# Performance work log

Measured on AMD Instinct MI355X. Metric: run time of the kernel, lower is better.

The kernel has to match this reference:

```python
import jax, jax.numpy as jnp
import numpy as np

D_MODEL = 1024
N_HEADS = 16
D_K = D_MODEL // N_HEADS
THETA = 10000.0
B, S = 2, 2048


def setup_inputs() -> dict:
    key = jax.random.key(0)
    ks = jax.random.split(key, 5)
    sigma = 2.0 / (D_MODEL + D_MODEL) ** 0.5
    x = jax.random.normal(ks[0], (B, S, D_MODEL), dtype=jnp.float32)
    Wq = jax.random.normal(ks[1], (D_MODEL, D_MODEL), dtype=jnp.float32) * sigma
    Wk = jax.random.normal(ks[2], (D_MODEL, D_MODEL), dtype=jnp.float32) * sigma
    Wv = jax.random.normal(ks[3], (D_MODEL, D_MODEL), dtype=jnp.float32) * sigma
    Wo = jax.random.normal(ks[4], (D_MODEL, D_MODEL), dtype=jnp.float32) * sigma
    token_positions = jnp.arange(S, dtype=jnp.int64 if jax.config.read('jax_enable_x64') else jnp.int32)
    return {"x": x, "Wq": Wq, "Wk": Wk, "Wv": Wv, "Wo": Wo, "token_positions": token_positions}


def _apply_rope(t, token_positions):
    # t: (H, B, S, D_K); token_positions: (S,) broadcasts over leading dims
    half = D_K // 2
    inv_freq = 1.0 / (THETA ** (jnp.arange(0, D_K, 2, dtype=jnp.float32) / D_K))  # (half,)
    ang = token_positions.astype(jnp.float32)[..., None] * inv_freq              # (S, half)
    cos, sin = jnp.cos(ang), jnp.sin(ang)
    t2 = t.reshape(*t.shape[:-1], half, 2)  # interleaved pairs
    o0 = t2[..., 0] * cos - t2[..., 1] * sin
    o1 = t2[..., 0] * sin + t2[..., 1] * cos
    return jnp.stack((o0, o1), axis=-1).reshape(t.shape)


def _split_heads(t):
    # (B, S, D_MODEL) -> (H, B, S, D_K)
    Bb, Ss, _ = t.shape
    return jnp.moveaxis(t.reshape(Bb, Ss, N_HEADS, D_K), 2, 0)


def reference(x, Wq, Wk, Wv, Wo, token_positions):
    Q = _split_heads(jnp.einsum('oi,bsi->bso', Wq, x))
    K = _split_heads(jnp.einsum('oi,bsi->bso', Wk, x))
    V = _split_heads(jnp.einsum('oi,bsi->bso', Wv, x))
    Q = _apply_rope(Q, token_positions)
    K = _apply_rope(K, token_positions)
    scores = jnp.einsum('hbqd,hbkd->hbqk', Q, K) * (D_K ** -0.5)  # (H,B,S,S)
    causal = jnp.tril(jnp.ones((S, S), dtype=bool))
    scores = jnp.where(causal, scores, -jnp.inf)
    attn = jax.nn.softmax(scores, axis=-1)
    out = jnp.einsum('hbqk,hbkd->hbqd', attn, V)  # (H,B,S,D_K)
    out = jnp.moveaxis(out, 0, 2).reshape(x.shape[0], x.shape[1], D_MODEL)
    return jnp.einsum('oi,bsi->bso', Wo, out)
```

## Files before the change

### kernel.cpp

```cpp
#include <hip/hip_runtime.h>

#define DM 1024
#define NH 16
#define DK 64
#define BB 2
#define SS 2048

typedef unsigned short u16;
typedef unsigned int   u32;
typedef __bf16 bf16x8 __attribute__((ext_vector_type(8)));
typedef float  f32x4  __attribute__((ext_vector_type(4)));
typedef float  f32x16 __attribute__((ext_vector_type(16)));

__device__ __forceinline__ u16 f2bf(float f){
  u32 u = __float_as_uint(f);
  u32 r = (u + 0x7FFFu + ((u >> 16) & 1u)) >> 16;
  return (u16)r;
}
__device__ __forceinline__ float bf2f(u16 v){ return __uint_as_float(((u32)v) << 16); }

__device__ __forceinline__ u32 cvtpk(float lo, float hi){
  u32 r;
  asm volatile("v_cvt_pk_bf16_f32 %0, %1, %2" : "=v"(r) : "v"(lo), "v"(hi));
  return r;
}

__device__ __forceinline__ void gl16(const void* g, void* l){
  __builtin_amdgcn_global_load_lds((const __attribute__((address_space(1))) u32*)g,
                                   (__attribute__((address_space(3))) u32*)l, 16, 0, 0);
}
__device__ __forceinline__ f32x4 mfma16(bf16x8 a, bf16x8 b, f32x4 c){
  return __builtin_amdgcn_mfma_f32_16x16x32_bf16(a, b, c, 0, 0, 0);
}
__device__ __forceinline__ f32x16 mfma32(bf16x8 a, bf16x8 b, f32x16 c){
  return __builtin_amdgcn_mfma_f32_32x32x16_bf16(a, b, c, 0, 0, 0);
}

__global__ void k_cast(const float* __restrict__ x,  const float* __restrict__ wq,
                       const float* __restrict__ wk, const float* __restrict__ wv,
                       const float* __restrict__ wo, u16* __restrict__ xb,
                       u16* __restrict__ wb, float* __restrict__ tab){
  if (blockIdx.x >= 8192){
    int e = (blockIdx.x - 8192)*256 + threadIdx.x;
    int p = e >> 5, j = e & 31;
    float s, c;
    sincosf((float)p * exp2f(-0.4152410118609203f * (float)j), &s, &c);
    float2 v; v.x = c; v.y = s;
    *(float2*)(tab + e*2) = v;
    return;
  }
  int e = blockIdx.x*1024 + threadIdx.x*4;
  int r = e >> 20;
  const float* s; u16* d; int local;
  if (r < 4){ s = x; d = xb; local = e; }
  else {
    const float* ws[4] = {wq, wk, wv, wo};
    int w = r - 4;
    local = e & 0xFFFFF;
    s = ws[w]; d = wb + ((size_t)w << 20);
  }
  float4 v = *(const float4*)(s + local);
  uint2 t; t.x = cvtpk(v.x, v.y); t.y = cvtpk(v.z, v.w);
  *(uint2*)(d + local) = t;
}

__device__ __forceinline__ int xcd_swz(int lin, int nwg){
  return (lin & 7) * (nwg >> 3) + (lin >> 3);
}

template<bool SWAP>
__device__ __forceinline__ void gemm_core(const u16* __restrict__ A, const u16* __restrict__ Bw,
                                          u16* S, f32x4 (&acc)[4][4], int m0, int n0){
  const int tid = threadIdx.x, lane = tid & 63, wid = tid >> 6;
  const int wm = (wid >> 1) * 64, wn = (wid & 1) * 64;
  const int ql = lane & 15, lg = lane >> 4;

  #define STAGE_G(buf, k0)                                                       \
    _Pragma("unroll")                                                            \
    for (int i = 0; i < 4; i++){                                                 \
      int L = i*4096 + tid*16;                                                   \
      int r_ = L >> 7;                                                           \
      int orig = ((L >> 4) & 7) ^ (r_ & 7);                                      \
      const u16* src = (orig < 4)                                                \
          ? (A  + (size_t)(m0 + r_)*DM + (k0) + orig*8)                          \
          : (Bw + (size_t)(n0 + r_)*DM + (k0) + (orig - 4)*8);                   \
      gl16(src, (char*)(buf) + L);                                               \
    }

  #define COMPUTE_T(buf)                                                         \
    {                                                                            \
      bf16x8 af[4], bfr[4];                                                      \
      _Pragma("unroll")                                                          \
      for (int mi = 0; mi < 4; mi++){                                            \
        int r = wm + mi*16 + ql;                                                 \
        af[mi] = *(const bf16x8*)((char*)(buf) + r*128 + ((lg*16) ^ ((r & 7) << 4))); \
      }                                                                          \
      _Pragma("unroll")                                                          \
      for (int ni = 0; ni < 4; ni++){                                            \
        int r = wn + ni*16 + ql;                                                 \
        bfr[ni] = *(const bf16x8*)((char*)(buf) + r*128 + ((64 + lg*16) ^ ((r & 7) << 4))); \
      }                                                                          \
      __builtin_amdgcn_s_setprio(1);                                             \
      _Pragma("unroll")                                                          \
      for (int mi = 0; mi < 4; mi++)                                             \
        _Pragma("unroll")                                                        \
        for (int ni = 0; ni < 4; ni++)                                           \
          acc[mi][ni] = SWAP ? mfma16(bfr[ni], af[mi], acc[mi][ni])              \
                             : mfma16(af[mi], bfr[ni], acc[mi][ni]);             \
      __builtin_amdgcn_s_setprio(0);                                             \
    }

  char* b0 = (char*)S;
  char* b1 = (char*)S + 16384;
  char* b2 = (char*)S + 32768;

  STAGE_G(b0, 0);
  STAGE_G(b1, 32);

  #pragma unroll 3
  for (int t = 0; t < 30; t++){
    asm volatile("s_waitcnt vmcnt(4)" ::: "memory");
    __builtin_amdgcn_s_barrier();
    STAGE_G(b2, (t+2)*32);
    COMPUTE_T(b0);
    char* tmp = b0; b0 = b1; b1 = b2; b2 = tmp;
  }
  asm volatile("s_waitcnt vmcnt(4)" ::: "memory");
  __builtin_amdgcn_s_barrier();
  COMPUTE_T(b0);
  { char* tmp = b0; b0 = b1; b1 = b2; b2 = tmp; }
  asm volatile("s_waitcnt vmcnt(0)" ::: "memory");
  __builtin_amdgcn_s_barrier();
  COMPUTE_T(b0);

  #undef STAGE_G
  #undef COMPUTE_T
}

__global__ __launch_bounds__(256) void k_gemm_qkv(const u16* __restrict__ xb, const u16* __restrict__ Wb,
                                                  u16* __restrict__ Qb, u16* __restrict__ Kb,
                                                  u16* __restrict__ Vt_g, const int* __restrict__ pos,
                                                  const float* __restrict__ tab){
  __shared__ __align__(16) u16 S[3*8192];
  int lin = (int)blockIdx.x + 8*((int)blockIdx.y + 32*(int)blockIdx.z);
  lin = xcd_swz(lin, 768);
  const int bx = lin & 7, by = (lin >> 3) & 31, z = lin >> 8;
  const int m0 = by * 128, n0 = bx * 128;

  const u16* Bw = Wb + ((size_t)z << 20);
  f32x4 acc[4][4] = {};
  gemm_core<true>(xb, Bw, S, acc, m0, n0);
  const int lane = threadIdx.x & 63, wid = threadIdx.x >> 6;
  const int wm0 = m0 + (wid >> 1)*64, wn0 = n0 + (wid & 1)*64;
  const int ql = lane & 15, lg = lane >> 4;

  if (z == 2){
    #pragma unroll
    for (int mi = 0; mi < 4; mi++){
      const int mrow = wm0 + mi*16 + ql;
      const int bq = mrow >> 11, sq = mrow & (SS-1);
      u16* vt = Vt_g + ((size_t)bq*NH*DK)*SS + sq;
      #pragma unroll
      for (int ni = 0; ni < 4; ni++){
        const int nb = wn0 + ni*16 + lg*4;
        #pragma unroll
        for (int r = 0; r < 4; r++)
          vt[(size_t)(nb + r)*SS] = f2bf(acc[mi][ni][r]);
      }
    }
    return;
  }

  u16* C = (z == 0) ? Qb : Kb;
  const float4* tab4 = (const float4*)tab;
  #pragma unroll
  for (int mi = 0; mi < 4; mi++){
    const int mrow = wm0 + mi*16 + ql;
    const int p = pos[mrow & (SS-1)];
    #pragma unroll
    for (int ni = 0; ni < 4; ni++){
      const int nb = wn0 + ni*16 + lg*4;
      float o0 = acc[mi][ni][0], o1 = acc[mi][ni][1];
      float o2 = acc[mi][ni][2], o3 = acc[mi][ni][3];
      int j0 = (nb >> 1) & 31;
      float4 cs = tab4[p*16 + (j0 >> 1)];
      float t0 = o0*cs.x - o1*cs.y, t1 = o0*cs.y + o1*cs.x;
      o0 = t0; o1 = t1;
      t0 = o2*cs.z - o3*cs.w; t1 = o2*cs.w + o3*cs.z;
      o2 = t0; o3 = t1;
      uint2 w; w.x = cvtpk(o0, o1); w.y = cvtpk(o2, o3);
      *(uint2*)(C + (size_t)mrow*DM + nb) = w;
    }
  }
}

__global__ __launch_bounds__(256) void k_gemm_out(const u16* __restrict__ AO, const u16* __restrict__ Wo,
                                                  float* __restrict__ Co){
  __shared__ __align__(16) u16 S[3*8192];
  int lin = (int)blockIdx.x + 8*(int)blockIdx.y;
  lin = xcd_swz(lin, 256);
  const int bx = lin & 7, by = lin >> 3;
  const int m0 = by * 128, n0 = bx * 128;

  f32x4 acc[4][4] = {};
  gemm_core<false>(AO, Wo, S, acc, m0, n0);
  const int lane = threadIdx.x & 63, wid = threadIdx.x >> 6;
  const int wm0 = m0 + (wid >> 1)*64, wn0 = n0 + (wid & 1)*64;
  #pragma unroll
  for (int mi = 0; mi < 4; mi++)
    #pragma unroll
    for (int ni = 0; ni < 4; ni++)
      #pragma unroll
      for (int r = 0; r < 4; r++){
        int m = wm0 + mi*16 + (lane >> 4)*4 + r;
        int n = wn0 + ni*16 + (lane & 15);
        Co[(size_t)m*DM + n] = acc[mi][ni][r];
      }
}

__global__ __launch_bounds__(512, 4) void k_attn(const u16* __restrict__ Q, const u16* __restrict__ K,
                                                 const u16* __restrict__ Vt_g, u16* __restrict__ AO){
  __shared__ __align__(16) u16 Ks[4][64*64];
  __shared__ __align__(16) u16 Vt[4][64*64];
  const int tid = threadIdx.x, lane = tid & 63, wid = tid >> 6;
  const int b = blockIdx.z, h = blockIdx.y;
  const int qb = b ? (15 - (int)blockIdx.x) : (int)blockIdx.x;
  const int strip = wid & 3, g = wid >> 2;
  const int qw = qb*128 + strip*32;
  const size_t base = ((size_t)b*SS)*DM + (size_t)h*DK;
  const size_t vtb  = ((size_t)b*NH + h)*DK*SS;
  const int qi = lane & 31, hh = lane >> 5;
  const int NI = qb + 1;
  const float SC = 0.18033688011112042f;
  const float THR = 8.0f / SC;
  const int qm15 = (qi & 15) << 4;

  const u16* qptr = Q + base + (size_t)(qw + qi)*DM + hh*8;
  bf16x8 qf0 = *(const bf16x8*)(qptr);
  bf16x8 qf1 = *(const bf16x8*)(qptr + 16);
  bf16x8 qf2 = *(const bf16x8*)(qptr + 32);
  bf16x8 qf3 = *(const bf16x8*)(qptr + 48);

  const int L = tid*16;
  const int Lm = ((L >> 3) & 0xF0) ^ ((L >> 6) & 0x10);
  const int A_ = L ^ Lm;
  const int srow = A_ >> 7;
  const int scol = (A_ & 127) >> 1;

  #define STAGE1(bi, t)                                                          \
    {                                                                             \
      const int kn0_ = (t)*64;                                                    \
      gl16(K    + base + (size_t)(kn0_ + srow)*DM + scol, (char*)Ks[bi] + L);      \
      gl16(Vt_g + vtb  + (size_t)srow*SS + kn0_ + scol, (char*)Vt[bi] + L);        \
    }

  STAGE1(0, 0); STAGE1(1, 1);
  if (NI > 1){
    STAGE1(2, 2); STAGE1(3, 3);
    asm volatile("s_waitcnt vmcnt(4)" ::: "memory");
  } else {
    asm volatile("s_waitcnt vmcnt(0)" ::: "memory");
  }
  __builtin_amdgcn_s_barrier();

  f32x16 oacc0 = {}, oacc1 = {};
  float m = -3e38f, lsum = 0.f;

  for (int k = 0; k < NI; k++){
    const int t = 2*k + g;
    const int kv0 = t*64;
    const int bsel = ((k & 1) << 1) | g;
    const char* kb = (const char*)Ks[bsel];
    const char* vb = (const char*)Vt[bsel];

    if (kv0 <= qw + 31){
      f32x16 sf0 = {}, sf1 = {};
      __builtin_amdgcn_s_setprio(1);
      #pragma unroll
      for (int kc = 0; kc < 4; kc++){
        const int co = kc*32 + hh*16;
        const int a0 = (qi*128 + co) ^ qm15;
        bf16x8 kfa = *(const bf16x8*)(kb + a0);
        bf16x8 kfb = *(const bf16x8*)(kb + a0 + 4096);
        bf16x8 qf = (kc == 0) ? qf0 : (kc == 1) ? qf1 : (kc == 2) ? qf2 : qf3;
        sf0 = mfma32(kfa, qf, sf0);
        sf1 = mfma32(kfb, qf, sf1);
      }
      __builtin_amdgcn_s_setprio(0);

      if (kv0 + 63 > qw){
        const int qa = qw + qi;
        #pragma unroll
        for (int r = 0; r < 16; r++){
          int rowoff = (r & 3) + 8*(r >> 2) + 4*hh;
          sf0[r] = (kv0 + rowoff      <= qa) ? sf0[r] : -3e38f;
          sf1[r] = (kv0 + 32 + rowoff <= qa) ? sf1[r] : -3e38f;
        }
      }

      float mx = -3e38f;
      #pragma unroll
      for (int r = 0; r < 16; r++) mx = fmaxf(mx, fmaxf(sf0[r], sf1[r]));
      if (!__all(mx <= m + THR)){
        mx = fmaxf(mx, __shfl_xor(mx, 32));
        const float mn = fmaxf(m, mx);
        const float alpha = exp2f((m - mn)*SC);
        oacc0 *= alpha; oacc1 *= alpha; lsum *= alpha;
        m = mn;
      }

      const float nms = -m*SC;
      float psum = 0.f;
      #pragma unroll
      for (int r = 0; r < 16; r++){
        sf0[r] = exp2f(fmaf(sf0[r], SC, nms));
        sf1[r] = exp2f(fmaf(sf1[r], SC, nms));
        psum += sf0[r] + sf1[r];
      }
      lsum += psum;

      __builtin_amdgcn_s_setprio(1);
      #define PVCHUNK(PS, TT, T4)                                                 \
        {                                                                         \
          u32 A0 = cvtpk(PS[8*(TT)+0], PS[8*(TT)+1]);                             \
          u32 A1 = cvtpk(PS[8*(TT)+2], PS[8*(TT)+3]);                             \
          u32 B0 = cvtpk(PS[8*(TT)+4], PS[8*(TT)+5]);                             \
          u32 B1 = cvtpk(PS[8*(TT)+6], PS[8*(TT)+7]);                             \
          u32 s0 = hh ? A0 : B0, s1 = hh ? A1 : B1;                               \
          u32 r0 = (u32)__shfl_xor((int)s0, 32);                                  \
          u32 r1 = (u32)__shfl_xor((int)s1, 32);                                  \
          u32 pw[4];                                                              \
          pw[0] = hh ? r0 : A0; pw[1] = hh ? r1 : A1;                             \
          pw[2] = hh ? B0 : r0; pw[3] = hh ? B1 : r1;                             \
          bf16x8 pf;                                                              \
          __builtin_memcpy(&pf, pw, 16);                                          \
          const int co = (T4)*32 + hh*16;                                         \
          const int av = (qi*128 + co) ^ qm15;                                    \
          bf16x8 vfa = *(const bf16x8*)(vb + av);                                 \
          bf16x8 vfb = *(const bf16x8*)(vb + av + 4096);                          \
          oacc0 = mfma32(vfa, pf, oacc0);                                         \
          oacc1 = mfma32(vfb, pf, oacc1);                                         \
        }
      PVCHUNK(sf0, 0, 0) PVCHUNK(sf0, 1, 1) PVCHUNK(sf1, 0, 2) PVCHUNK(sf1, 1, 3)
      #undef PVCHUNK
      __builtin_amdgcn_s_setprio(0);
    }

    __builtin_amdgcn_s_barrier();
    if (k + 2 < NI){
      STAGE1(((k & 1) << 1) | 0, 2*k + 4);
      STAGE1(((k & 1) << 1) | 1, 2*k + 5);
    }
    if (k + 1 < NI){
      if (k + 2 < NI) asm volatile("s_waitcnt vmcnt(4)" ::: "memory");
      else            asm volatile("s_waitcnt vmcnt(0)" ::: "memory");
      __builtin_amdgcn_s_barrier();
    }
  }
  #undef STAGE1

  __builtin_amdgcn_s_barrier();
  float2* exv  = (float2*)Ks;
  float2* exml = (float2*)((char*)Vt + 16384);
  if (g == 1){
    int idx = (wid - 4)*64 + lane;
    #pragma unroll
    for (int e = 0; e < 8; e++){
      float2 v0; v0.x = oacc0[2*e]; v0.y = oacc0[2*e+1];
      float2 v1; v1.x = oacc1[2*e]; v1.y = oacc1[2*e+1];
      exv[e*256 + idx] = v0;
      exv[(8+e)*256 + idx] = v1;
    }
    float2 ml; ml.x = m; ml.y = lsum;
    exml[idx] = ml;
  }
  __builtin_amdgcn_s_barrier();
  if (g == 1) return;

  {
    int idx = wid*64 + lane;
    float2 ml = exml[idx];
    const float mm = fmaxf(m, ml.x);
    const float aA = exp2f((m - mm)*SC);
    const float aB = exp2f((ml.x - mm)*SC);
    lsum = lsum*aA + ml.y*aB;
    #pragma unroll
    for (int e = 0; e < 8; e++){
      float2 v0 = exv[e*256 + idx];
      float2 v1 = exv[(8+e)*256 + idx];
      oacc0[2*e]   = oacc0[2*e]*aA   + v0.x*aB;
      oacc0[2*e+1] = oacc0[2*e+1]*aA + v0.y*aB;
      oacc1[2*e]   = oacc1[2*e]*aA   + v1.x*aB;
      oacc1[2*e+1] = oacc1[2*e+1]*aA + v1.y*aB;
    }
  }
  lsum += __shfl_xor(lsum, 32);
  const float rl = 1.0f / lsum;

  char* sc = (char*)Vt[0] + wid*4096;
  #pragma unroll
  for (int w = 0; w < 8; w++){
    const int pb = (w & 1)*2 + (w >> 1)*8;
    const int db0 = 4*hh + pb;
    const int db1 = 32 + 4*hh + pb;
    *(u32*)(sc + ((qi*128 + db0*2) ^ ((qi & 7) << 4))) = cvtpk(oacc0[2*w]*rl, oacc0[2*w+1]*rl);
    *(u32*)(sc + ((qi*128 + db1*2) ^ ((qi & 7) << 4))) = cvtpk(oacc1[2*w]*rl, oacc1[2*w+1]*rl);
  }
  #pragma unroll
  for (int pass = 0; pass < 4; pass++){
    int qr = pass*8 + (lane >> 3);
    int d0 = (lane & 7)*8;
    bf16x8 row = *(const bf16x8*)(sc + ((qr*128 + d0*2) ^ ((qr & 7) << 4)));
    *(bf16x8*)(AO + base + (size_t)(qw + qr)*DM + d0) = row;
  }
}

extern "C" void kernel_launch(void* const* d_in, const int* in_sizes, int n_in,
                              void* d_out, int out_size, void* d_ws, size_t ws_size,
                              hipStream_t stream){
  const float* x   = (const float*)d_in[0];
  const float* Wq  = (const float*)d_in[1];
  const float* Wk  = (const float*)d_in[2];
  const float* Wv  = (const float*)d_in[3];
  const float* Wo  = (const float*)d_in[4];
  const int*   pos = (const int*)d_in[5];
  float* out = (float*)d_out;

  const size_t NEED = ((size_t)41 << 20);
  if (ws_size < NEED){
    hipMemsetAsync(d_out, 0x7f, (size_t)out_size * sizeof(float), stream);
    return;
  }

  char* ws = (char*)d_ws;
  u16* xb   = (u16*)(ws);
  u16* Wb   = (u16*)(ws + ((size_t)8  << 20));
  u16* Qb   = (u16*)(ws + ((size_t)16 << 20));
  u16* Kb   = (u16*)(ws + ((size_t)24 << 20));
  u16* Vt   = (u16*)(ws + ((size_t)32 << 20));
  float* tab = (float*)(ws + ((size_t)40 << 20));
  u16* AO = xb;

  k_cast<<<8448, 256, 0, stream>>>(x, Wq, Wk, Wv, Wo, xb, Wb, tab);
  k_gemm_qkv<<<dim3(8, 32, 3), 256, 0, stream>>>(xb, Wb, Qb, Kb, Vt, pos, tab);
  k_attn<<<dim3(16, 16, 2), 512, 0, stream>>>(Qb, Kb, Vt, AO);
  k_gemm_out<<<dim3(8, 32), 256, 0, stream>>>(AO, Wb + ((size_t)3 << 20), out);
}
```

Baseline: 110.1 us.

## Split attention KV tile into two 32-row halves with permlane32 swap

Restructures the inner attention loop to process each 64-key tile as two 32-key halves, each with its own QK MFMA, online-softmax update and PV MFMAs. This roughly halves live score registers and lets per-half causal masking skip fully visible halves. The cross-half-wave P exchange now uses v_permlane32_swap instead of ds_bpermute-based shfl_xor plus selects, and the max reduction becomes a tree. The cost is two softmax rescale checks per tile instead of one, and shorter MFMA chains that may hide latency less well.

After: 109.2 us (median of 2 runs). Within noise of the previous version (-0.8%).

```diff
diff --git a/kernel.cpp b/kernel.cpp
--- a/kernel.cpp
+++ b/kernel.cpp
@@ -274,76 +274,72 @@
     const char* vb = (const char*)Vt[bsel];
 
     if (kv0 <= qw + 31){
-      f32x16 sf0 = {}, sf1 = {};
-      __builtin_amdgcn_s_setprio(1);
       #pragma unroll
-      for (int kc = 0; kc < 4; kc++){
-        const int co = kc*32 + hh*16;
-        const int a0 = (qi*128 + co) ^ qm15;
-        bf16x8 kfa = *(const bf16x8*)(kb + a0);
-        bf16x8 kfb = *(const bf16x8*)(kb + a0 + 4096);
-        bf16x8 qf = (kc == 0) ? qf0 : (kc == 1) ? qf1 : (kc == 2) ? qf2 : qf3;
-        sf0 = mfma32(kfa, qf, sf0);
-        sf1 = mfma32(kfb, qf, sf1);
-      }
-      __builtin_amdgcn_s_setprio(0);
-
-      if (kv0 + 63 > qw){
-        const int qa = qw + qi;
+      for (int H = 0; H < 2; H++){
+        f32x16 sf = {};
+        __builtin_amdgcn_s_setprio(1);
+        #pragma unroll
+        for (int kc = 0; kc < 4; kc++){
+          const int a0 = (qi*128 + kc*32 + hh*16) ^ qm15;
+          bf16x8 kf = *(const bf16x8*)(kb + a0 + H*4096);
+          bf16x8 qf = (kc == 0) ? qf0 : (kc == 1) ? qf1 : (kc == 2) ? qf2 : qf3;
+          sf = mfma32(kf, qf, sf);
+        }
+        __builtin_amdgcn_s_setprio(0);
+
+        if (kv0 + 32*H + 31 > qw){
+          const int qa = qw + qi;
+          #pragma unroll
+          for (int r = 0; r < 16; r++){
+            int rowoff = 32*H + (r & 3) + 8*(r >> 2) + 4*hh;
+            sf[r] = (kv0 + rowoff <= qa) ? sf[r] : -3e38f;
+          }
+        }
+
+        float t0 = fmaxf(fmaxf(sf[0],  sf[1]),  sf[2]);
+        float t1 = fmaxf(fmaxf(sf[3],  sf[4]),  sf[5]);
+        float t2 = fmaxf(fmaxf(sf[6],  sf[7]),  sf[8]);
+        float t3 = fmaxf(fmaxf(sf[9],  sf[10]), sf[11]);
+        float t4 = fmaxf(fmaxf(sf[12], sf[13]), sf[14]);
+        float mx = fmaxf(fmaxf(fmaxf(t0, t1), t2), fmaxf(fmaxf(t3, t4), sf[15]));
+
+        if (!__all(mx <= m + THR)){
+          mx = fmaxf(mx, __shfl_xor(mx, 32));
+          const float mn = fmaxf(m, mx);
+          const float alpha = exp2f((m - mn)*SC);
+          oacc0 *= alpha; oacc1 *= alpha; lsum *= alpha;
+          m = mn;
+        }
+
+        const float nms = -m*SC;
+        float psum = 0.f;
         #pragma unroll
         for (int r = 0; r < 16; r++){
-          int rowoff = (r & 3) + 8*(r >> 2) + 4*hh;
-          sf0[r] = (kv0 + rowoff      <= qa) ? sf0[r] : -3e38f;
-          sf1[r] = (kv0 + 32 + rowoff <= qa) ? sf1[r] : -3e38f;
+          sf[r] = exp2f(fmaf(sf[r], SC, nms));
+          psum += sf[r];
         }
+        lsum += psum;
+
+        __builtin_amdgcn_s_setprio(1);
+        #pragma unroll
+        for (int TT = 0; TT < 2; TT++){
+          u32 w0 = cvtpk(sf[8*TT+0], sf[8*TT+1]);
+          u32 w1 = cvtpk(sf[8*TT+2], sf[8*TT+3]);
+          u32 w2 = cvtpk(sf[8*TT+4], sf[8*TT+5]);
+          u32 w3 = cvtpk(sf[8*TT+6], sf[8*TT+7]);
+          asm volatile("v_permlane32_swap_b32 %0, %1" : "+v"(w0), "+v"(w2));
+          asm volatile("v_permlane32_swap_b32 %0, %1" : "+v"(w1), "+v"(w3));
+          u32 pw[4] = {w0, w1, w2, w3};
+          bf16x8 pf;
+          __builtin_memcpy(&pf, pw, 16);
+          const int av = (qi*128 + (2*H + TT)*32 + hh*16) ^ qm15;
+          bf16x8 vfa = *(const bf16x8*)(vb + av);
+          bf16x8 vfb = *(const bf16x8*)(vb + av + 4096);
+          oacc0 = mfma32(vfa, pf, oacc0);
+          oacc1 = mfma32(vfb, pf, oacc1);
+        }
+        __builtin_amdgcn_s_setprio(0);
       }
-
-      float mx = -3e38f;
-      #pragma unroll
-      for (int r = 0; r < 16; r++) mx = fmaxf(mx, fmaxf(sf0[r], sf1[r]));
-      if (!__all(mx <= m + THR)){
-        mx = fmaxf(mx, __shfl_xor(mx, 32));
-        const float mn = fmaxf(m, mx);
-        const float alpha = exp2f((m - mn)*SC);
-        oacc0 *= alpha; oacc1 *= alpha; lsum *= alpha;
-        m = mn;
-      }
-
-      const float nms = -m*SC;
-      float psum = 0.f;
-      #pragma unroll
-      for (int r = 0; r < 16; r++){
-        sf0[r] = exp2f(fmaf(sf0[r], SC, nms));
-        sf1[r] = exp2f(fmaf(sf1[r], SC, nms));
-        psum += sf0[r] + sf1[r];
-      }
-      lsum += psum;
-
-      __builtin_amdgcn_s_setprio(1);
-      #define PVCHUNK(PS, TT, T4)                                                 \
-        {                                                                         \
-          u32 A0 = cvtpk(PS[8*(TT)+0], PS[8*(TT)+1]);                             \
-          u32 A1 = cvtpk(PS[8*(TT)+2], PS[8*(TT)+3]);                             \
-          u32 B0 = cvtpk(PS[8*(TT)+4], PS[8*(TT)+5]);                             \
-          u32 B1 = cvtpk(PS[8*(TT)+6], PS[8*(TT)+7]);                             \
-          u32 s0 = hh ? A0 : B0, s1 = hh ? A1 : B1;                               \
-          u32 r0 = (u32)__shfl_xor((int)s0, 32);                                  \
-          u32 r1 = (u32)__shfl_xor((int)s1, 32);                                  \
-          u32 pw[4];                                                              \
-          pw[0] = hh ? r0 : A0; pw[1] = hh ? r1 : A1;                             \
-          pw[2] = hh ? B0 : r0; pw[3] = hh ? B1 : r1;                             \
-          bf16x8 pf;                                                              \
-          __builtin_memcpy(&pf, pw, 16);                                          \
-          const int co = (T4)*32 + hh*16;                                         \
-          const int av = (qi*128 + co) ^ qm15;                                    \
-          bf16x8 vfa = *(const bf16x8*)(vb + av);                                 \
-          bf16x8 vfb = *(const bf16x8*)(vb + av + 4096);                          \
-          oacc0 = mfma32(vfa, pf, oacc0);                                         \
-          oacc1 = mfma32(vfb, pf, oacc1);                                         \
-        }
-      PVCHUNK(sf0, 0, 0) PVCHUNK(sf0, 1, 1) PVCHUNK(sf1, 0, 2) PVCHUNK(sf1, 1, 3)
-      #undef PVCHUNK
-      __builtin_amdgcn_s_setprio(0);
     }
 
     __builtin_amdgcn_s_barrier();
```
